# Kernel optimization log

Hardware: AMD Instinct MI355X
Metric: run time of the kernel (lower is better)

The kernel has to match this reference:

```python
import jax, jax.numpy as jnp
import numpy as np

D_MODEL = 1024
ED = 2048        # d_inner = expand_factor * d_model
N = 16           # d_state
DT_RANK = 64     # ceil(d_model/16)
K = 4            # d_conv
B_SZ = 4
L = 512


def _causal_depthwise_conv(u, w, b):
    # u: [B, L, ED], w: [ED, 1, K], b: [ED]
    xc = jnp.transpose(u, (0, 2, 1))  # [B, ED, L]
    xc = jax.lax.conv_general_dilated(
        xc, w, window_strides=(1,), padding=[(K - 1, 0)],
        feature_group_count=ED, dimension_numbers=('NCH', 'OIH', 'NCH'))
    xc = xc + b[None, :, None]
    return jnp.transpose(xc, (0, 2, 1))  # [B, L, ED]


def _ssm_branch(xz_half, z, conv_w, conv_b, Wx, Wdt, b_dt, A_log, Dp):
    # xz_half, z: [B, L, ED]
    x = jax.nn.silu(_causal_depthwise_conv(xz_half, conv_w, conv_b))
    dbc = x @ Wx.T  # [B, L, dt_rank + 2N]
    delta = dbc[..., :DT_RANK]
    Bm = dbc[..., DT_RANK:DT_RANK + N]
    Cm = dbc[..., DT_RANK + N:]
    delta = jax.nn.softplus(delta @ Wdt.T + b_dt)  # [B, L, ED]
    A = -jnp.exp(A_log)  # [ED, N]
    dA = jnp.exp(delta[..., None] * A)                        # [B, L, ED, N]
    bx = (delta[..., None] * Bm[:, :, None, :]) * x[..., None]  # [B, L, ED, N]
    dA_t = jnp.transpose(dA, (1, 0, 2, 3))
    bx_t = jnp.transpose(bx, (1, 0, 2, 3))
    c_t = jnp.transpose(Cm, (1, 0, 2))  # [L, B, N]
    h0 = jnp.zeros((x.shape[0], ED, N), dtype=x.dtype)

    def step(h, inp):
        dAi, bxi, ci = inp
        h = dAi * h + bxi
        return h, jnp.einsum('ben,bn->be', h, ci)

    _, ys = jax.lax.scan(step, h0, (dA_t, bx_t, c_t))
    y = jnp.transpose(ys, (1, 0, 2)) + Dp * x  # D skip connection
    return y * jax.nn.silu(z)                  # gate


def _mamba_block(x, W_in, conv_w, conv_b, Wx, Wdt, b_dt, A_log, Dp,
                 conv_w_b, conv_b_b, Wx_b, Wdt_b, b_dt_b, A_log_b, Dp_b, W_out):
    xz = x @ W_in.T  # [B, L, 2*ED]
    xf, zf = xz[..., :ED], xz[..., ED:]
    y = _ssm_branch(xf, zf, conv_w, conv_b, Wx, Wdt, b_dt, A_log, Dp)
    xz_r = xz[:, ::-1, :]
    xb, zb = xz_r[..., :ED], xz_r[..., ED:]
    y_b = _ssm_branch(xb, zb, conv_w_b, conv_b_b, Wx_b, Wdt_b, b_dt_b, A_log_b, Dp_b)
    y = (y + y_b[:, ::-1, :]) * 0.5
    return y @ W_out.T


def setup_inputs() -> dict:
    key = jax.random.key(0)
    ks = jax.random.split(key, 20)
    s = lambda k, shp, sc: jax.random.normal(k, shp, dtype=jnp.float32) * sc
    dt = jnp.exp(jax.random.uniform(ks[15], (ED,)) * (np.log(0.1) - np.log(0.001)) + np.log(0.001))
    dt = jnp.clip(dt, 1e-4, None)
    inv_dt = dt + jnp.log(-jnp.expm1(-dt))
    A_init = jnp.log(jnp.tile(jnp.arange(1, N + 1, dtype=jnp.float32), (ED, 1)))
    return {
        'x': s(ks[0], (B_SZ, L, D_MODEL), 1.0),
        'W_in': s(ks[1], (2 * ED, D_MODEL), D_MODEL ** -0.5),
        'conv_w': s(ks[2], (ED, 1, K), K ** -0.5),
        'conv_b': s(ks[3], (ED,), 0.02),
        'Wx': s(ks[4], (DT_RANK + 2 * N, ED), ED ** -0.5),
        'Wdt': jax.random.uniform(ks[5], (ED, DT_RANK), minval=-DT_RANK ** -0.5, maxval=DT_RANK ** -0.5),
        'b_dt': inv_dt,
        'A_log': A_init,
        'Dp': jnp.ones((ED,), dtype=jnp.float32),
        'conv_w_b': s(ks[6], (ED, 1, K), K ** -0.5),
        'conv_b_b': s(ks[7], (ED,), 0.02),
        'Wx_b': s(ks[8], (DT_RANK + 2 * N, ED), ED ** -0.5),
        'Wdt_b': jax.random.uniform(ks[9], (ED, DT_RANK), minval=-DT_RANK ** -0.5, maxval=DT_RANK ** -0.5),
        'b_dt_b': inv_dt,
        'A_log_b': A_init,
        'Dp_b': jnp.ones((ED,), dtype=jnp.float32),
        'W_out': s(ks[10], (D_MODEL, ED), ED ** -0.5),
    }


def reference(x, W_in, conv_w, conv_b, Wx, Wdt, b_dt, A_log, Dp,
              conv_w_b, conv_b_b, Wx_b, Wdt_b, b_dt_b, A_log_b, Dp_b, W_out):
    return _mamba_block(x, W_in, conv_w, conv_b, Wx, Wdt, b_dt, A_log, Dp,
                        conv_w_b, conv_b_b, Wx_b, Wdt_b, b_dt_b, A_log_b, Dp_b, W_out)
```

## Files before the change

kernel.cpp:

```cpp
#include <hip/hip_runtime.h>
#include <hip/hip_bf16.h>
#include <stdint.h>

typedef unsigned short ushort_t;
typedef __attribute__((ext_vector_type(8))) short short8;
typedef __attribute__((ext_vector_type(4))) float f32x4;
typedef __attribute__((ext_vector_type(2))) float f32x2;

__device__ __forceinline__ float b2f(ushort_t u) {
    union { uint32_t i; float f; } v; v.i = ((uint32_t)u) << 16; return v.f;
}
__device__ __forceinline__ ushort_t f2b(float f) {
    union { float f; uint32_t i; } v; v.f = f;
    uint32_t r = v.i + 0x7fff + ((v.i >> 16) & 1);
    return (ushort_t)(r >> 16);
}

#if __has_builtin(__builtin_amdgcn_exp2f)
#define EXP2(x) __builtin_amdgcn_exp2f(x)
#else
#define EXP2(x) __expf((x) * 0.69314718056f)
#endif

__device__ __forceinline__ void ll16(const ushort_t* g, ushort_t* l) {
    __builtin_amdgcn_global_load_lds(
        (const __attribute__((address_space(1))) uint32_t*)g,
        (__attribute__((address_space(3))) uint32_t*)l, 16, 0, 0);
}

template <int CTRL>
__device__ __forceinline__ float dpp_add(float p) {
    int v = __builtin_amdgcn_update_dpp(0, __float_as_int(p), CTRL, 0xF, 0xF, true);
    return p + __int_as_float(v);
}
#define DPP_XOR1 0xB1
#define DPP_XOR2 0x4E
#define DPP_HMIR 0x141

__device__ __forceinline__ void epi_wave_f32(
    float* sw, const f32x4* accg, float* dst0, int ldc, int lane)
{
    const int quad = lane >> 4, lr = lane & 15;
#pragma unroll
    for (int j = 0; j < 4; j++)
#pragma unroll
        for (int r = 0; r < 4; r++)
            sw[(quad * 4 + r) * 64 + j * 16 + lr] = accg[j][r];
    __asm__ volatile("s_waitcnt lgkmcnt(0)" ::: "memory");
#pragma unroll
    for (int t = 0; t < 4; t++) {
        int row = t * 4 + quad;
        float4 v = *(const float4*)(&sw[row * 64 + lr * 4]);
        *(float4*)(dst0 + (size_t)row * ldc + lr * 4) = v;
    }
}

__device__ __forceinline__ void epi_wave_b16(
    float* sw, const f32x4* accg, ushort_t* dst0, int ldc, int lane)
{
    const int quad = lane >> 4, lr = lane & 15;
#pragma unroll
    for (int j = 0; j < 4; j++)
#pragma unroll
        for (int r = 0; r < 4; r++)
            sw[(quad * 4 + r) * 64 + j * 16 + lr] = accg[j][r];
    __asm__ volatile("s_waitcnt lgkmcnt(0)" ::: "memory");
#pragma unroll
    for (int t = 0; t < 4; t++) {
        int row = t * 4 + quad;
        float4 v = *(const float4*)(&sw[row * 64 + lr * 4]);
        ushort4 o; o.x = f2b(v.x); o.y = f2b(v.y); o.z = f2b(v.z); o.w = f2b(v.w);
        *(ushort4*)(dst0 + (size_t)row * ldc + lr * 4) = o;
    }
}

struct CastSeg { const float4* src; ushort4* dst; };
struct CastArgs { CastSeg seg[7]; int start[8]; };

__global__ __launch_bounds__(256) void cast_multi(CastArgs a)
{
    int g = blockIdx.x * 256 + threadIdx.x;
    if (g >= a.start[7]) return;
    int s = 0;
#pragma unroll
    for (int i = 1; i < 7; i++) s += (g >= a.start[i]);
    int i = g - a.start[s];
    float4 v = a.seg[s].src[i];
    ushort4 o;
    o.x = f2b(v.x); o.y = f2b(v.y); o.z = f2b(v.z); o.w = f2b(v.w);
    a.seg[s].dst[i] = o;
}

#define BK 32

__global__ __launch_bounds__(256) void gemm_g1(
    const ushort_t* __restrict__ A, int lda,
    const ushort_t* __restrict__ B, int ldb,
    ushort_t* __restrict__ Cout, int ldc, int Kd)
{
    __shared__ ushort_t As[128 * BK];
    __shared__ ushort_t Bs[128 * BK];
    __shared__ float sepi[4][1024];

    const int tid  = threadIdx.x;
    const int m0   = blockIdx.y * 128;
    const int n0   = blockIdx.x * 128;
    const int wv   = tid >> 6;
    const int lane = tid & 63;
    const int wm   = (wv >> 1) * 64;
    const int wn   = (wv & 1) * 64;
    const int lr   = lane & 15;
    const int quad = lane >> 4;

    f32x4 acc[4][4];
#pragma unroll
    for (int i = 0; i < 4; i++)
#pragma unroll
        for (int j = 0; j < 4; j++) acc[i][j] = f32x4{0.f, 0.f, 0.f, 0.f};

    const int srA = wv * 32 + (lane >> 2);
    const int scA = (lane & 3) * 8;

    for (int k0 = 0; k0 < Kd; k0 += BK) {
        ll16(A + (size_t)(m0 + srA) * lda + k0 + scA,      &As[wv * 1024]);
        ll16(A + (size_t)(m0 + srA + 16) * lda + k0 + scA, &As[wv * 1024 + 512]);
        ll16(B + (size_t)(n0 + srA) * ldb + k0 + scA,      &Bs[wv * 1024]);
        ll16(B + (size_t)(n0 + srA + 16) * ldb + k0 + scA, &Bs[wv * 1024 + 512]);
        __syncthreads();

        short8 af[4], bf[4];
#pragma unroll
        for (int i = 0; i < 4; i++)
            af[i] = *(const short8*)(&As[(wm + i * 16 + lr) * BK + quad * 8]);
#pragma unroll
        for (int j = 0; j < 4; j++)
            bf[j] = *(const short8*)(&Bs[(wn + j * 16 + lr) * BK + quad * 8]);
#pragma unroll
        for (int i = 0; i < 4; i++)
#pragma unroll
            for (int j = 0; j < 4; j++)
                acc[i][j] = __builtin_amdgcn_mfma_f32_16x16x32_bf16(af[i], bf[j], acc[i][j], 0, 0, 0);
        __syncthreads();
    }

#pragma unroll
    for (int g = 0; g < 4; g++)
        epi_wave_b16(sepi[wv], acc[g],
                     Cout + (size_t)(m0 + wm + g * 16) * ldc + n0 + wn, ldc, lane);
}

__global__ __launch_bounds__(256) void gemm_g4(
    const ushort_t* __restrict__ A, int lda,
    const ushort_t* __restrict__ B, int ldb,
    float* __restrict__ Cout, int ldc, int Kd)
{
    __shared__ ushort_t As[64 * BK];
    __shared__ ushort_t Bs[128 * BK];
    __shared__ float sepi[4][1024];

    const int tid  = threadIdx.x;
    const int m0   = blockIdx.y * 64;
    const int n0   = blockIdx.x * 128;
    const int wv   = tid >> 6;
    const int lane = tid & 63;
    const int wm   = (wv >> 1) * 32;
    const int wn   = (wv & 1) * 64;
    const int lr   = lane & 15;
    const int quad = lane >> 4;

    f32x4 acc[2][4];
#pragma unroll
    for (int i = 0; i < 2; i++)
#pragma unroll
        for (int j = 0; j < 4; j++) acc[i][j] = f32x4{0.f, 0.f, 0.f, 0.f};

    const int srA = wv * 16 + (lane >> 2);
    const int srB = wv * 32 + (lane >> 2);
    const int sc  = (lane & 3) * 8;

    for (int k0 = 0; k0 < Kd; k0 += BK) {
        ll16(A + (size_t)(m0 + srA) * lda + k0 + sc,      &As[wv * 512]);
        ll16(B + (size_t)(n0 + srB) * ldb + k0 + sc,      &Bs[wv * 1024]);
        ll16(B + (size_t)(n0 + srB + 16) * ldb + k0 + sc, &Bs[wv * 1024 + 512]);
        __syncthreads();

        short8 af[2], bf[4];
#pragma unroll
        for (int i = 0; i < 2; i++)
            af[i] = *(const short8*)(&As[(wm + i * 16 + lr) * BK + quad * 8]);
#pragma unroll
        for (int j = 0; j < 4; j++)
            bf[j] = *(const short8*)(&Bs[(wn + j * 16 + lr) * BK + quad * 8]);
#pragma unroll
        for (int i = 0; i < 2; i++)
#pragma unroll
            for (int j = 0; j < 4; j++)
                acc[i][j] = __builtin_amdgcn_mfma_f32_16x16x32_bf16(af[i], bf[j], acc[i][j], 0, 0, 0);
        __syncthreads();
    }

#pragma unroll
    for (int g = 0; g < 2; g++)
        epi_wave_f32(sepi[wv], acc[g],
                     Cout + (size_t)(m0 + wm + g * 16) * ldc + n0 + wn, ldc, lane);
}

__global__ __launch_bounds__(256) void gemm_g2(
    const ushort_t* __restrict__ xc, const ushort_t* __restrict__ wx,
    float* __restrict__ part)
{
    __shared__ ushort_t As[128 * BK];
    __shared__ ushort_t Bs[128 * BK];
    __shared__ float sepi[4][1024];

    const int sk = blockIdx.x, mb = blockIdx.y, br = blockIdx.z;
    const ushort_t* A = xc + (size_t)br * 2048 * 2048;
    const ushort_t* B = wx + (size_t)br * 96 * 2048;
    float* C = part + (size_t)(sk * 2 + br) * 2048 * 96;
    const int m0 = mb * 128;
    const int kb = sk * 256;

    const int tid  = threadIdx.x;
    const int wv   = tid >> 6;
    const int lane = tid & 63;
    const int wm   = (wv >> 1) * 64;
    const int wn   = (wv & 1) * 64;
    const int lr   = lane & 15;
    const int quad = lane >> 4;

    f32x4 acc[4][4];
#pragma unroll
    for (int i = 0; i < 4; i++)
#pragma unroll
        for (int j = 0; j < 4; j++) acc[i][j] = f32x4{0.f, 0.f, 0.f, 0.f};

    const int srA = wv * 32 + (lane >> 2);
    const int sc  = (lane & 3) * 8;

    for (int k0 = kb; k0 < kb + 256; k0 += BK) {
        ll16(A + (size_t)(m0 + srA) * 2048 + k0 + sc,      &As[wv * 1024]);
        ll16(A + (size_t)(m0 + srA + 16) * 2048 + k0 + sc, &As[wv * 1024 + 512]);
        ll16(B + (size_t)(srA) * 2048 + k0 + sc,           &Bs[wv * 1024]);
        ll16(B + (size_t)(srA + 16) * 2048 + k0 + sc,      &Bs[wv * 1024 + 512]);
        __syncthreads();

        short8 af[4], bf[4];
#pragma unroll
        for (int i = 0; i < 4; i++)
            af[i] = *(const short8*)(&As[(wm + i * 16 + lr) * BK + quad * 8]);
#pragma unroll
        for (int j = 0; j < 4; j++)
            bf[j] = *(const short8*)(&Bs[(wn + j * 16 + lr) * BK + quad * 8]);
#pragma unroll
        for (int i = 0; i < 4; i++)
#pragma unroll
            for (int j = 0; j < 4; j++)
                acc[i][j] = __builtin_amdgcn_mfma_f32_16x16x32_bf16(af[i], bf[j], acc[i][j], 0, 0, 0);
        __syncthreads();
    }

    float* sw = sepi[wv];
#pragma unroll
    for (int g = 0; g < 4; g++) {
#pragma unroll
        for (int j = 0; j < 4; j++)
#pragma unroll
            for (int r = 0; r < 4; r++)
                sw[(quad * 4 + r) * 64 + j * 16 + lr] = acc[g][j][r];
        __asm__ volatile("s_waitcnt lgkmcnt(0)" ::: "memory");
        int col = wn + lr * 4;
#pragma unroll
        for (int t = 0; t < 4; t++) {
            int row = t * 4 + quad;
            if (col < 96) {
                float4 v = *(const float4*)(&sw[row * 64 + lr * 4]);
                *(float4*)(C + (size_t)(m0 + wm + g * 16 + row) * 96 + col) = v;
            }
        }
    }
}

__global__ __launch_bounds__(256) void reduce_dbc(
    const float4* __restrict__ part, ushort4* __restrict__ dbc16)
{
    int g = blockIdx.x * 256 + threadIdx.x;
    const int S = 2 * 2048 * 96 / 4;
    float4 r = part[g];
#pragma unroll
    for (int i = 1; i < 8; i++) {
        float4 p = part[g + i * S];
        r.x += p.x; r.y += p.y; r.z += p.z; r.w += p.w;
    }
    ushort4 o; o.x = f2b(r.x); o.y = f2b(r.y); o.z = f2b(r.z); o.w = f2b(r.w);
    dbc16[g] = o;
}

__global__ __launch_bounds__(256) void gemm_g3(
    const ushort_t* __restrict__ dbc16, const ushort_t* __restrict__ wdt,
    ushort_t* __restrict__ delta,
    const float* __restrict__ bdt_f, const float* __restrict__ bdt_b)
{
    __shared__ ushort_t As[128 * BK];
    __shared__ ushort_t Bs[128 * BK];
    __shared__ float sepi[4][1024];

    const int br = blockIdx.z;
    const ushort_t* A = dbc16 + (size_t)br * 2048 * 96;
    const ushort_t* B = wdt + (size_t)br * 2048 * 64;
    ushort_t* C = delta + (size_t)br * 2048 * 2048;
    const float* bias = br ? bdt_b : bdt_f;

    const int tid  = threadIdx.x;
    const int m0   = blockIdx.y * 128;
    const int n0   = blockIdx.x * 128;
    const int wv   = tid >> 6;
    const int lane = tid & 63;
    const int wm   = (wv >> 1) * 64;
    const int wn   = (wv & 1) * 64;
    const int lr   = lane & 15;
    const int quad = lane >> 4;

    f32x4 acc[4][4];
#pragma unroll
    for (int i = 0; i < 4; i++)
#pragma unroll
        for (int j = 0; j < 4; j++) acc[i][j] = f32x4{0.f, 0.f, 0.f, 0.f};

    const int srA = wv * 32 + (lane >> 2);
    const int sc  = (lane & 3) * 8;

    for (int k0 = 0; k0 < 64; k0 += BK) {
        ll16(A + (size_t)(m0 + srA) * 96 + k0 + sc,       &As[wv * 1024]);
        ll16(A + (size_t)(m0 + srA + 16) * 96 + k0 + sc,  &As[wv * 1024 + 512]);
        ll16(B + (size_t)(n0 + srA) * 64 + k0 + sc,       &Bs[wv * 1024]);
        ll16(B + (size_t)(n0 + srA + 16) * 64 + k0 + sc,  &Bs[wv * 1024 + 512]);
        __syncthreads();

        short8 af[4], bf[4];
#pragma unroll
        for (int i = 0; i < 4; i++)
            af[i] = *(const short8*)(&As[(wm + i * 16 + lr) * BK + quad * 8]);
#pragma unroll
        for (int j = 0; j < 4; j++)
            bf[j] = *(const short8*)(&Bs[(wn + j * 16 + lr) * BK + quad * 8]);
#pragma unroll
        for (int i = 0; i < 4; i++)
#pragma unroll
            for (int j = 0; j < 4; j++)
                acc[i][j] = __builtin_amdgcn_mfma_f32_16x16x32_bf16(af[i], bf[j], acc[i][j], 0, 0, 0);
        __syncthreads();
    }

    float bn[4];
#pragma unroll
    for (int j = 0; j < 4; j++) bn[j] = bias[n0 + wn + j * 16 + lr];
#pragma unroll
    for (int g = 0; g < 4; g++)
#pragma unroll
        for (int j = 0; j < 4; j++)
#pragma unroll
            for (int r = 0; r < 4; r++) {
                float x = acc[g][j][r] + bn[j];
                float sp = fmaxf(x, 0.f) + __logf(1.f + __expf(-fabsf(x)));
                acc[g][j][r] = sp;
            }

#pragma unroll
    for (int g = 0; g < 4; g++)
        epi_wave_b16(sepi[wv], acc[g],
                     C + (size_t)(m0 + wm + g * 16) * 2048 + n0 + wn, 2048, lane);
}

__global__ __launch_bounds__(256) void conv_silu_kernel(
    const ushort_t* __restrict__ xz,
    const float* __restrict__ w_f, const float* __restrict__ cb_f,
    const float* __restrict__ w_b, const float* __restrict__ cb_b,
    ushort_t* __restrict__ xc16)
{
    int g = blockIdx.x * 256 + threadIdx.x;
    int e  = g & 2047;
    int t  = (g >> 11) & 511;
    int b  = (g >> 20) & 3;
    int br = g >> 22;

    const float* w  = br ? w_b  : w_f;
    const float* cb = br ? cb_b : cb_f;

    float acc = cb[e];
    float4 wv = *(const float4*)(w + e * 4);
    float wk[4] = { wv.x, wv.y, wv.z, wv.w };

#pragma unroll
    for (int k = 0; k < 4; k++) {
        int tp = t - 3 + k;
        if (tp >= 0) {
            int row = br ? (511 - tp) : tp;
            acc += wk[k] * b2f(xz[((size_t)(b * 512 + row)) * 4096 + e]);
        }
    }
    float s = acc / (1.f + __expf(-acc));
    xc16[g] = f2b(s);
}

__global__ __launch_bounds__(256, 4) void scan_kernel(
    const ushort_t* __restrict__ delta,
    const ushort_t* __restrict__ xc,
    const ushort_t* __restrict__ dbc16,
    const ushort_t* __restrict__ xz,
    const float* __restrict__ Alog_f, const float* __restrict__ Alog_b,
    const float* __restrict__ Dp_f,   const float* __restrict__ Dp_b,
    ushort_t* __restrict__ yf, ushort_t* __restrict__ yb)
{
    const int blk = blockIdx.x;
    const int eg = blk & 63;
    const int b  = (blk >> 6) & 3;
    const int br = blk >> 8;
    const int e0 = eg * 32;

    const int tid = threadIdx.x;
    const int n2  = tid & 7;
    const int el  = tid >> 3;
    const int e   = e0 + el;

    const float* Alog = br ? Alog_b : Alog_f;
    const float* Dpp  = br ? Dp_b   : Dp_f;
    f32x2 a01;
    a01.x = -__expf(Alog[e * 16 + n2]) * 1.44269504f;
    a01.y = -__expf(Alog[e * 16 + n2 + 8]) * 1.44269504f;

    size_t tb = ((size_t)br * 4 + b) * 512;
    const ushort_t* dlt  = delta + tb * 2048;
    const ushort_t* xcb  = xc    + tb * 2048;
    const ushort_t* dbcb = dbc16 + tb * 96;
    ushort_t* y = (br ? yb : yf) + (size_t)b * 512 * 2048;

    __shared__ float sd [2][32][36];
    __shared__ float sdx[2][32][36];
    __shared__ float sBp[2][8][34][2];
    __shared__ float sCp[2][8][34][2];
    __shared__ float sy [2][32][33];

    const int stt = tid >> 3;
    const int seg = tid & 7;
    const int sg4 = seg * 4;

    float4 rD = *(const float4*)(Dpp + e0 + sg4);

    uint2 rdx, rx, rbc, rz;
    uint2 rx_c, rx_f, rz_c, rz_f;

    auto load_regs = [&](int c) {
        int row = c * 32 + stt;
        rdx = *(const uint2*)(dlt + (size_t)row * 2048 + e0 + sg4);
        rx  = *(const uint2*)(xcb + (size_t)row * 2048 + e0 + sg4);
        rbc = *(const uint2*)(dbcb + (size_t)row * 96 + 64 + sg4);
        int orow = br ? (511 - row) : row;
        rz  = *(const uint2*)(xz + ((size_t)(b * 512 + orow)) * 4096 + 2048 + e0 + sg4);
    };
    auto write_lds = [&](int buf) {
        const uint32_t dw[2] = { rdx.x, rdx.y };
        const uint32_t xw[2] = { rx.x, rx.y };
#pragma unroll
        for (int k = 0; k < 2; k++) {
            float d0 = b2f((ushort_t)(dw[k] & 0xffff));
            float d1 = b2f((ushort_t)(dw[k] >> 16));
            float x0 = b2f((ushort_t)(xw[k] & 0xffff));
            float x1 = b2f((ushort_t)(xw[k] >> 16));
            sd [buf][sg4 + 2 * k][stt]     = d0;
            sd [buf][sg4 + 2 * k + 1][stt] = d1;
            sdx[buf][sg4 + 2 * k][stt]     = d0 * x0;
            sdx[buf][sg4 + 2 * k + 1][stt] = d1 * x1;
        }
        float* arr = (seg < 4) ? &sBp[buf][0][0][0] : &sCp[buf][0][0][0];
        const int nb = (seg & 3) * 4;
        const uint32_t bw[2] = { rbc.x, rbc.y };
#pragma unroll
        for (int k = 0; k < 2; k++) {
            int na = nb + 2 * k, nbd = nb + 2 * k + 1;
            arr[(na  & 7) * 68 + stt * 2 + (na  >> 3)] = b2f((ushort_t)(bw[k] & 0xffff));
            arr[(nbd & 7) * 68 + stt * 2 + (nbd >> 3)] = b2f((ushort_t)(bw[k] >> 16));
        }
    };
    auto flush = [&](int cm1) {
        const int bufm1 = cm1 & 1;
        int row = cm1 * 32 + stt;
        const uint32_t zw[2] = { rz_f.x, rz_f.y };
        float zv[4];
#pragma unroll
        for (int k = 0; k < 2; k++) {
            zv[2 * k]     = b2f((ushort_t)(zw[k] & 0xffff));
            zv[2 * k + 1] = b2f((ushort_t)(zw[k] >> 16));
        }
        float pv[4];
#pragma unroll
        for (int k = 0; k < 4; k++) pv[k] = sy[bufm1][stt][sg4 + k];
        const uint32_t xw[2] = { rx_f.x, rx_f.y };
        float xvv[4];
#pragma unroll
        for (int k = 0; k < 2; k++) {
            xvv[2 * k]     = b2f((ushort_t)(xw[k] & 0xffff));
            xvv[2 * k + 1] = b2f((ushort_t)(xw[k] >> 16));
        }
        const float Dv[4] = { rD.x, rD.y, rD.z, rD.w };
        uint32_t op[2];
#pragma unroll
        for (int k = 0; k < 2; k++) {
            float ga = (pv[2 * k]     + Dv[2 * k]     * xvv[2 * k])     *
                       (zv[2 * k]     / (1.f + __expf(-zv[2 * k])));
            float gb = (pv[2 * k + 1] + Dv[2 * k + 1] * xvv[2 * k + 1]) *
                       (zv[2 * k + 1] / (1.f + __expf(-zv[2 * k + 1])));
            op[k] = (uint32_t)f2b(ga) | ((uint32_t)f2b(gb) << 16);
        }
        *(uint2*)(y + (size_t)row * 2048 + e0 + sg4) = make_uint2(op[0], op[1]);
    };

    f32x2 h01 = f32x2{0.f, 0.f};

    load_regs(0);
    write_lds(0);
    rx_c = rx; rz_c = rz;

    for (int c = 0; c < 16; ++c) {
        if (c < 15) load_regs(c + 1);
        __syncthreads();
        const int buf = c & 1;

        auto LDQ = [&](int tq, f32x4& dv, f32x4& dxv, f32x4& bq0, f32x4& bq1,
                       f32x4& cq0, f32x4& cq1) {
            dv  = *(const f32x4*)(&sd [buf][el][tq]);
            dxv = *(const f32x4*)(&sdx[buf][el][tq]);
            bq0 = *(const f32x4*)(&sBp[buf][n2][tq][0]);
            bq1 = *(const f32x4*)(&sBp[buf][n2][tq + 2][0]);
            cq0 = *(const f32x4*)(&sCp[buf][n2][tq][0]);
            cq1 = *(const f32x4*)(&sCp[buf][n2][tq + 2][0]);
        };

        f32x4 dv_p, dxv_p, bq0_p, bq1_p, cq0_p, cq1_p;
        LDQ(0, dv_p, dxv_p, bq0_p, bq1_p, cq0_p, cq1_p);

        float pout[4];
#pragma unroll 4
        for (int tq = 0; tq < 32; tq += 4) {
            const f32x4 dv = dv_p, dxv = dxv_p;
            const f32x4 bq0 = bq0_p, bq1 = bq1_p, cq0 = cq0_p, cq1 = cq1_p;
            LDQ((tq + 4) & 31, dv_p, dxv_p, bq0_p, bq1_p, cq0_p, cq1_p);

#define SSTEP(DC, DXC, BT, CT, TI)                                   \
            {                                                        \
                f32x2 arg = a01 * (DC);                              \
                f32x2 ee; ee.x = EXP2(arg.x); ee.y = EXP2(arg.y);    \
                h01 = ee * h01 + (BT) * (DXC);                       \
                f32x2 pp = h01 * (CT);                               \
                float p = pp.x + pp.y;                               \
                p = dpp_add<DPP_XOR1>(p);                            \
                p = dpp_add<DPP_XOR2>(p);                            \
                p = dpp_add<DPP_HMIR>(p);                            \
                pout[TI] = p;                                        \
            }
            SSTEP(dv.x, dxv.x, bq0.xy, cq0.xy, 0)
            SSTEP(dv.y, dxv.y, bq0.zw, cq0.zw, 1)
            SSTEP(dv.z, dxv.z, bq1.xy, cq1.xy, 2)
            SSTEP(dv.w, dxv.w, bq1.zw, cq1.zw, 3)
#undef SSTEP

            if (n2 == 0) {
                sy[buf][tq + 0][el] = pout[0];
                sy[buf][tq + 1][el] = pout[1];
                sy[buf][tq + 2][el] = pout[2];
                sy[buf][tq + 3][el] = pout[3];
            }
        }

        if (c > 0) flush(c - 1);

        if (c < 15) {
            write_lds((c + 1) & 1);
            rx_f = rx_c; rz_f = rz_c;
            rx_c = rx;   rz_c = rz;
        } else {
            rx_f = rx_c; rz_f = rz_c;
        }
    }
    __syncthreads();
    flush(15);
}

__global__ __launch_bounds__(256) void combine_kernel(
    const uint2* __restrict__ yf, const uint2* __restrict__ yb,
    uint2* __restrict__ yc)
{
    int g = blockIdx.x * 256 + threadIdx.x;
    int e4 = g & 511;
    int t  = (g >> 9) & 511;
    int b  = g >> 18;
    uint2 a = yf[g];
    uint2 c = yb[((size_t)(b * 512 + 511 - t)) * 512 + e4];
    uint2 o;
    o.x = (uint32_t)f2b(0.5f * (b2f((ushort_t)(a.x & 0xffff)) + b2f((ushort_t)(c.x & 0xffff)))) |
          ((uint32_t)f2b(0.5f * (b2f((ushort_t)(a.x >> 16)) + b2f((ushort_t)(c.x >> 16)))) << 16);
    o.y = (uint32_t)f2b(0.5f * (b2f((ushort_t)(a.y & 0xffff)) + b2f((ushort_t)(c.y & 0xffff)))) |
          ((uint32_t)f2b(0.5f * (b2f((ushort_t)(a.y >> 16)) + b2f((ushort_t)(c.y >> 16)))) << 16);
    yc[g] = o;
}

static const size_t TT = 2048;
static const size_t OFF_XZ16  = 0;
static const size_t OFF_XC16  = OFF_XZ16  + TT*4096*2;
static const size_t OFF_DBC16 = OFF_XC16  + 2*TT*2048*2;
static const size_t OFF_DELTA = OFF_DBC16 + 2*TT*96*2;
static const size_t OFF_YF    = OFF_DELTA + 2*TT*2048*2;
static const size_t OFF_YB    = OFF_YF    + TT*2048*2;
static const size_t OFF_YC16  = OFF_YB    + TT*2048*2;
static const size_t OFF_X16   = OFF_YC16  + TT*2048*2;
static const size_t OFF_WIN16 = OFF_X16   + TT*1024*2;
static const size_t OFF_WX16  = OFF_WIN16 + 4096*1024*2;
static const size_t OFF_WDT16 = OFF_WX16  + 2*96*2048*2;
static const size_t OFF_WOUT16= OFF_WDT16 + 2*2048*64*2;
static const size_t OFF_PART  = OFF_WOUT16+ 1024*2048*2;

extern "C" void kernel_launch(void* const* d_in, const int* in_sizes, int n_in,
                              void* d_out, int out_size, void* d_ws, size_t ws_size,
                              hipStream_t stream) {
    const float* x       = (const float*)d_in[0];
    const float* W_in    = (const float*)d_in[1];
    const float* conv_w  = (const float*)d_in[2];
    const float* conv_b  = (const float*)d_in[3];
    const float* Wx      = (const float*)d_in[4];
    const float* Wdt     = (const float*)d_in[5];
    const float* b_dt    = (const float*)d_in[6];
    const float* A_log   = (const float*)d_in[7];
    const float* Dp      = (const float*)d_in[8];
    const float* conv_w_b= (const float*)d_in[9];
    const float* conv_b_b= (const float*)d_in[10];
    const float* Wx_b    = (const float*)d_in[11];
    const float* Wdt_b   = (const float*)d_in[12];
    const float* b_dt_b  = (const float*)d_in[13];
    const float* A_log_b = (const float*)d_in[14];
    const float* Dp_b    = (const float*)d_in[15];
    const float* W_out   = (const float*)d_in[16];
    float* out = (float*)d_out;

    char* ws = (char*)d_ws;
    ushort_t* xz16  = (ushort_t*)(ws + OFF_XZ16);
    ushort_t* xc16  = (ushort_t*)(ws + OFF_XC16);
    ushort_t* dbc16 = (ushort_t*)(ws + OFF_DBC16);
    ushort_t* delta = (ushort_t*)(ws + OFF_DELTA);
    ushort_t* yf    = (ushort_t*)(ws + OFF_YF);
    ushort_t* yb    = (ushort_t*)(ws + OFF_YB);
    ushort_t* yc16  = (ushort_t*)(ws + OFF_YC16);
    ushort_t* x16   = (ushort_t*)(ws + OFF_X16);
    ushort_t* win16 = (ushort_t*)(ws + OFF_WIN16);
    ushort_t* wx16  = (ushort_t*)(ws + OFF_WX16);
    ushort_t* wdt16 = (ushort_t*)(ws + OFF_WDT16);
    ushort_t* wout16= (ushort_t*)(ws + OFF_WOUT16);
    float*    part  = (float*)(ws + OFF_PART);

    dim3 blk(256);

    CastArgs ca;
    const int n4s[7] = {524288, 1048576, 49152, 49152, 32768, 32768, 524288};
    ca.seg[0] = { (const float4*)x,     (ushort4*)x16 };
    ca.seg[1] = { (const float4*)W_in,  (ushort4*)win16 };
    ca.seg[2] = { (const float4*)Wx,    (ushort4*)wx16 };
    ca.seg[3] = { (const float4*)Wx_b,  (ushort4*)(wx16 + 96 * 2048) };
    ca.seg[4] = { (const float4*)Wdt,   (ushort4*)wdt16 };
    ca.seg[5] = { (const float4*)Wdt_b, (ushort4*)(wdt16 + 2048 * 64) };
    ca.seg[6] = { (const float4*)W_out, (ushort4*)wout16 };
    ca.start[0] = 0;
    for (int i = 0; i < 7; i++) ca.start[i + 1] = ca.start[i] + n4s[i];
    cast_multi<<<(ca.start[7] + 255) / 256, blk, 0, stream>>>(ca);

    gemm_g1<<<dim3(32, 16), blk, 0, stream>>>(x16, 1024, win16, 1024, xz16, 4096, 1024);

    conv_silu_kernel<<<32768, blk, 0, stream>>>(xz16, conv_w, conv_b, conv_w_b, conv_b_b, xc16);

    gemm_g2<<<dim3(8, 16, 2), blk, 0, stream>>>(xc16, wx16, part);
    reduce_dbc<<<384, blk, 0, stream>>>((const float4*)part, (ushort4*)dbc16);

    gemm_g3<<<dim3(16, 16, 2), blk, 0, stream>>>(dbc16, wdt16, delta, b_dt, b_dt_b);

    scan_kernel<<<512, blk, 0, stream>>>(delta, xc16, dbc16, xz16, A_log, A_log_b, Dp, Dp_b, yf, yb);

    combine_kernel<<<4096, blk, 0, stream>>>((const uint2*)yf, (const uint2*)yb, (uint2*)yc16);

    gemm_g4<<<dim3(8, 32), blk, 0, stream>>>(yc16, 2048, wout16, 2048, out, 1024, 2048);
}
```

Measured before the change: 274.0 us.

## Double-buffer LDS tiles in GEMM kernels and XOR-swizzle scan LDS layout

Converts the four MFMA GEMM kernels to double-buffered LDS staging, so the next K-tile is loaded while the current one is computed and one barrier per iteration is dropped. Separately, it XOR-swizzles the column index of the delta and delta*x shared arrays in the scan kernel to reduce LDS bank conflicts on the transposed writes. Double buffering doubles the A/B LDS footprint, which may lower occupancy. Whether the loads actually overlap depends on how ll16 issues them.

```diff
diff --git a/kernel.cpp b/kernel.cpp
--- a/kernel.cpp
+++ b/kernel.cpp
@@ -98,8 +98,8 @@
     const ushort_t* __restrict__ B, int ldb,
     ushort_t* __restrict__ Cout, int ldc, int Kd)
 {
-    __shared__ ushort_t As[128 * BK];
-    __shared__ ushort_t Bs[128 * BK];
+    __shared__ ushort_t As[2][128 * BK];
+    __shared__ ushort_t Bs[2][128 * BK];
     __shared__ float sepi[4][1024];
 
     const int tid  = threadIdx.x;
@@ -121,25 +121,33 @@
     const int srA = wv * 32 + (lane >> 2);
     const int scA = (lane & 3) * 8;
 
-    for (int k0 = 0; k0 < Kd; k0 += BK) {
-        ll16(A + (size_t)(m0 + srA) * lda + k0 + scA,      &As[wv * 1024]);
-        ll16(A + (size_t)(m0 + srA + 16) * lda + k0 + scA, &As[wv * 1024 + 512]);
-        ll16(B + (size_t)(n0 + srA) * ldb + k0 + scA,      &Bs[wv * 1024]);
-        ll16(B + (size_t)(n0 + srA + 16) * ldb + k0 + scA, &Bs[wv * 1024 + 512]);
-        __syncthreads();
-
-        short8 af[4], bf[4];
+    auto stage = [&](int bf_, int k0) {
+        ll16(A + (size_t)(m0 + srA) * lda + k0 + scA,      &As[bf_][wv * 1024]);
+        ll16(A + (size_t)(m0 + srA + 16) * lda + k0 + scA, &As[bf_][wv * 1024 + 512]);
+        ll16(B + (size_t)(n0 + srA) * ldb + k0 + scA,      &Bs[bf_][wv * 1024]);
+        ll16(B + (size_t)(n0 + srA + 16) * ldb + k0 + scA, &Bs[bf_][wv * 1024 + 512]);
+    };
+
+    const int nk = Kd / BK;
+    stage(0, 0);
+    __syncthreads();
+
+    for (int t = 0; t < nk; ++t) {
+        const int buf = t & 1;
+        if (t + 1 < nk) stage(buf ^ 1, (t + 1) * BK);
+
+        short8 af[4], bfr[4];
 #pragma unroll
         for (int i = 0; i < 4; i++)
-            af[i] = *(const short8*)(&As[(wm + i * 16 + lr) * BK + quad * 8]);
+            af[i] = *(const short8*)(&As[buf][(wm + i * 16 + lr) * BK + quad * 8]);
 #pragma unroll
         for (int j = 0; j < 4; j++)
-            bf[j] = *(const short8*)(&Bs[(wn + j * 16 + lr) * BK + quad * 8]);
+            bfr[j] = *(const short8*)(&Bs[buf][(wn + j * 16 + lr) * BK + quad * 8]);
 #pragma unroll
         for (int i = 0; i < 4; i++)
 #pragma unroll
             for (int j = 0; j < 4; j++)
-                acc[i][j] = __builtin_amdgcn_mfma_f32_16x16x32_bf16(af[i], bf[j], acc[i][j], 0, 0, 0);
+                acc[i][j] = __builtin_amdgcn_mfma_f32_16x16x32_bf16(af[i], bfr[j], acc[i][j], 0, 0, 0);
         __syncthreads();
     }
 
@@ -154,8 +162,8 @@
     const ushort_t* __restrict__ B, int ldb,
     float* __restrict__ Cout, int ldc, int Kd)
 {
-    __shared__ ushort_t As[64 * BK];
-    __shared__ ushort_t Bs[128 * BK];
+    __shared__ ushort_t As[2][64 * BK];
+    __shared__ ushort_t Bs[2][128 * BK];
     __shared__ float sepi[4][1024];
 
     const int tid  = threadIdx.x;
@@ -178,24 +186,32 @@
     const int srB = wv * 32 + (lane >> 2);
     const int sc  = (lane & 3) * 8;
 
-    for (int k0 = 0; k0 < Kd; k0 += BK) {
-        ll16(A + (size_t)(m0 + srA) * lda + k0 + sc,      &As[wv * 512]);
-        ll16(B + (size_t)(n0 + srB) * ldb + k0 + sc,      &Bs[wv * 1024]);
-        ll16(B + (size_t)(n0 + srB + 16) * ldb + k0 + sc, &Bs[wv * 1024 + 512]);
-        __syncthreads();
-
-        short8 af[2], bf[4];
+    auto stage = [&](int bf_, int k0) {
+        ll16(A + (size_t)(m0 + srA) * lda + k0 + sc,      &As[bf_][wv * 512]);
+        ll16(B + (size_t)(n0 + srB) * ldb + k0 + sc,      &Bs[bf_][wv * 1024]);
+        ll16(B + (size_t)(n0 + srB + 16) * ldb + k0 + sc, &Bs[bf_][wv * 1024 + 512]);
+    };
+
+    const int nk = Kd / BK;
+    stage(0, 0);
+    __syncthreads();
+
+    for (int t = 0; t < nk; ++t) {
+        const int buf = t & 1;
+        if (t + 1 < nk) stage(buf ^ 1, (t + 1) * BK);
+
+        short8 af[2], bfr[4];
 #pragma unroll
         for (int i = 0; i < 2; i++)
-            af[i] = *(const short8*)(&As[(wm + i * 16 + lr) * BK + quad * 8]);
+            af[i] = *(const short8*)(&As[buf][(wm + i * 16 + lr) * BK + quad * 8]);
 #pragma unroll
         for (int j = 0; j < 4; j++)
-            bf[j] = *(const short8*)(&Bs[(wn + j * 16 + lr) * BK + quad * 8]);
+            bfr[j] = *(const short8*)(&Bs[buf][(wn + j * 16 + lr) * BK + quad * 8]);
 #pragma unroll
         for (int i = 0; i < 2; i++)
 #pragma unroll
             for (int j = 0; j < 4; j++)
-                acc[i][j] = __builtin_amdgcn_mfma_f32_16x16x32_bf16(af[i], bf[j], acc[i][j], 0, 0, 0);
+                acc[i][j] = __builtin_amdgcn_mfma_f32_16x16x32_bf16(af[i], bfr[j], acc[i][j], 0, 0, 0);
         __syncthreads();
     }
 
@@ -209,8 +225,8 @@
     const ushort_t* __restrict__ xc, const ushort_t* __restrict__ wx,
     float* __restrict__ part)
 {
-    __shared__ ushort_t As[128 * BK];
-    __shared__ ushort_t Bs[128 * BK];
+    __shared__ ushort_t As[2][128 * BK];
+    __shared__ ushort_t Bs[2][128 * BK];
     __shared__ float sepi[4][1024];
 
     const int sk = blockIdx.x, mb = blockIdx.y, br = blockIdx.z;
@@ -237,25 +253,32 @@
     const int srA = wv * 32 + (lane >> 2);
     const int sc  = (lane & 3) * 8;
 
-    for (int k0 = kb; k0 < kb + 256; k0 += BK) {
-        ll16(A + (size_t)(m0 + srA) * 2048 + k0 + sc,      &As[wv * 1024]);
-        ll16(A + (size_t)(m0 + srA + 16) * 2048 + k0 + sc, &As[wv * 1024 + 512]);
-        ll16(B + (size_t)(srA) * 2048 + k0 + sc,           &Bs[wv * 1024]);
-        ll16(B + (size_t)(srA + 16) * 2048 + k0 + sc,      &Bs[wv * 1024 + 512]);
-        __syncthreads();
-
-        short8 af[4], bf[4];
+    auto stage = [&](int bf_, int k0) {
+        ll16(A + (size_t)(m0 + srA) * 2048 + k0 + sc,      &As[bf_][wv * 1024]);
+        ll16(A + (size_t)(m0 + srA + 16) * 2048 + k0 + sc, &As[bf_][wv * 1024 + 512]);
+        ll16(B + (size_t)(srA) * 2048 + k0 + sc,           &Bs[bf_][wv * 1024]);
+        ll16(B + (size_t)(srA + 16) * 2048 + k0 + sc,      &Bs[bf_][wv * 1024 + 512]);
+    };
+
+    stage(0, kb);
+    __syncthreads();
+
+    for (int t = 0; t < 8; ++t) {
+        const int buf = t & 1;
+        if (t + 1 < 8) stage(buf ^ 1, kb + (t + 1) * BK);
+
+        short8 af[4], bfr[4];
 #pragma unroll
         for (int i = 0; i < 4; i++)
-            af[i] = *(const short8*)(&As[(wm + i * 16 + lr) * BK + quad * 8]);
+            af[i] = *(const short8*)(&As[buf][(wm + i * 16 + lr) * BK + quad * 8]);
 #pragma unroll
         for (int j = 0; j < 4; j++)
-            bf[j] = *(const short8*)(&Bs[(wn + j * 16 + lr) * BK + quad * 8]);
+            bfr[j] = *(const short8*)(&Bs[buf][(wn + j * 16 + lr) * BK + quad * 8]);
 #pragma unroll
         for (int i = 0; i < 4; i++)
 #pragma unroll
             for (int j = 0; j < 4; j++)
-                acc[i][j] = __builtin_amdgcn_mfma_f32_16x16x32_bf16(af[i], bf[j], acc[i][j], 0, 0, 0);
+                acc[i][j] = __builtin_amdgcn_mfma_f32_16x16x32_bf16(af[i], bfr[j], acc[i][j], 0, 0, 0);
         __syncthreads();
     }
 
@@ -300,8 +323,8 @@
     ushort_t* __restrict__ delta,
     const float* __restrict__ bdt_f, const float* __restrict__ bdt_b)
 {
-    __shared__ ushort_t As[128 * BK];
-    __shared__ ushort_t Bs[128 * BK];
+    __shared__ ushort_t As[2][128 * BK];
+    __shared__ ushort_t Bs[2][128 * BK];
     __shared__ float sepi[4][1024];
 
     const int br = blockIdx.z;
@@ -329,25 +352,32 @@
     const int srA = wv * 32 + (lane >> 2);
     const int sc  = (lane & 3) * 8;
 
-    for (int k0 = 0; k0 < 64; k0 += BK) {
-        ll16(A + (size_t)(m0 + srA) * 96 + k0 + sc,       &As[wv * 1024]);
-        ll16(A + (size_t)(m0 + srA + 16) * 96 + k0 + sc,  &As[wv * 1024 + 512]);
-        ll16(B + (size_t)(n0 + srA) * 64 + k0 + sc,       &Bs[wv * 1024]);
-        ll16(B + (size_t)(n0 + srA + 16) * 64 + k0 + sc,  &Bs[wv * 1024 + 512]);
-        __syncthreads();
-
-        short8 af[4], bf[4];
+    auto stage = [&](int bf_, int k0) {
+        ll16(A + (size_t)(m0 + srA) * 96 + k0 + sc,       &As[bf_][wv * 1024]);
+        ll16(A + (size_t)(m0 + srA + 16) * 96 + k0 + sc,  &As[bf_][wv * 1024 + 512]);
+        ll16(B + (size_t)(n0 + srA) * 64 + k0 + sc,       &Bs[bf_][wv * 1024]);
+        ll16(B + (size_t)(n0 + srA + 16) * 64 + k0 + sc,  &Bs[bf_][wv * 1024 + 512]);
+    };
+
+    stage(0, 0);
+    __syncthreads();
+
+    for (int t = 0; t < 2; ++t) {
+        const int buf = t & 1;
+        if (t + 1 < 2) stage(buf ^ 1, (t + 1) * BK);
+
+        short8 af[4], bfr[4];
 #pragma unroll
         for (int i = 0; i < 4; i++)
-            af[i] = *(const short8*)(&As[(wm + i * 16 + lr) * BK + quad * 8]);
+            af[i] = *(const short8*)(&As[buf][(wm + i * 16 + lr) * BK + quad * 8]);
 #pragma unroll
         for (int j = 0; j < 4; j++)
-            bf[j] = *(const short8*)(&Bs[(wn + j * 16 + lr) * BK + quad * 8]);
+            bfr[j] = *(const short8*)(&Bs[buf][(wn + j * 16 + lr) * BK + quad * 8]);
 #pragma unroll
         for (int i = 0; i < 4; i++)
 #pragma unroll
             for (int j = 0; j < 4; j++)
-                acc[i][j] = __builtin_amdgcn_mfma_f32_16x16x32_bf16(af[i], bf[j], acc[i][j], 0, 0, 0);
+                acc[i][j] = __builtin_amdgcn_mfma_f32_16x16x32_bf16(af[i], bfr[j], acc[i][j], 0, 0, 0);
         __syncthreads();
     }
 
@@ -443,6 +473,7 @@
     const int stt = tid >> 3;
     const int seg = tid & 7;
     const int sg4 = seg * 4;
+    const int sdk = (seg & 3) * 8;
 
     float4 rD = *(const float4*)(Dpp + e0 + sg4);
 
@@ -460,16 +491,17 @@
     auto write_lds = [&](int buf) {
         const uint32_t dw[2] = { rdx.x, rdx.y };
         const uint32_t xw[2] = { rx.x, rx.y };
+        const int col = stt ^ sdk;
 #pragma unroll
         for (int k = 0; k < 2; k++) {
             float d0 = b2f((ushort_t)(dw[k] & 0xffff));
             float d1 = b2f((ushort_t)(dw[k] >> 16));
             float x0 = b2f((ushort_t)(xw[k] & 0xffff));
             float x1 = b2f((ushort_t)(xw[k] >> 16));
-            sd [buf][sg4 + 2 * k][stt]     = d0;
-            sd [buf][sg4 + 2 * k + 1][stt] = d1;
-            sdx[buf][sg4 + 2 * k][stt]     = d0 * x0;
-            sdx[buf][sg4 + 2 * k + 1][stt] = d1 * x1;
+            sd [buf][sg4 + 2 * k][col]     = d0;
+            sd [buf][sg4 + 2 * k + 1][col] = d1;
+            sdx[buf][sg4 + 2 * k][col]     = d0 * x0;
+            sdx[buf][sg4 + 2 * k + 1][col] = d1 * x1;
         }
         float* arr = (seg < 4) ? &sBp[buf][0][0][0] : &sCp[buf][0][0][0];
         const int nb = (seg & 3) * 4;
@@ -515,6 +547,7 @@
     };
 
     f32x2 h01 = f32x2{0.f, 0.f};
+    const int elk = ((el >> 2) & 3) * 8;
 
     load_regs(0);
     write_lds(0);
@@ -527,8 +560,9 @@
 
         auto LDQ = [&](int tq, f32x4& dv, f32x4& dxv, f32x4& bq0, f32x4& bq1,
                        f32x4& cq0, f32x4& cq1) {
-            dv  = *(const f32x4*)(&sd [buf][el][tq]);
-            dxv = *(const f32x4*)(&sdx[buf][el][tq]);
+            const int tc = tq ^ elk;
+            dv  = *(const f32x4*)(&sd [buf][el][tc]);
+            dxv = *(const f32x4*)(&sdx[buf][el][tc]);
             bq0 = *(const f32x4*)(&sBp[buf][n2][tq][0]);
             bq1 = *(const f32x4*)(&sBp[buf][n2][tq + 2][0]);
             cq0 = *(const f32x4*)(&sCp[buf][n2][tq][0]);
```

New measurement: 271.2 us. No clear change (-1.0%).
